# Performance work log

Hardware: AMD Instinct MI355X
Metric: run time of the kernel (lower is better)

Reference implementation:

```python
import jax, jax.numpy as jnp
import numpy as np

VOCAB, EMB, HID = 32000, 64, 64
B, S = 16, 256


def setup_inputs() -> dict:
    key = jax.random.key(0)
    ks = jax.random.split(key, 8)
    sc_e = 1.0  # torch nn.Embedding default init is N(0,1)
    sc = 1.0 / np.sqrt(HID)
    emb = jax.random.normal(ks[0], (VOCAB, EMB), jnp.float32) * sc_e
    emb = emb.at[0].set(0.0)  # padding_idx=0
    tokens = jax.random.randint(ks[1], (B, S), 0, VOCAB)
    w_ih = jax.random.normal(ks[2], (3 * HID, EMB), jnp.float32) * sc
    w_hh = jax.random.normal(ks[3], (3 * HID, HID), jnp.float32) * sc
    b_ih = jax.random.normal(ks[4], (3 * HID,), jnp.float32) * sc
    b_hh = jax.random.normal(ks[5], (3 * HID,), jnp.float32) * sc
    w_out = jax.random.normal(ks[6], (VOCAB, HID), jnp.float32) * sc
    b_out = jax.random.normal(ks[7], (VOCAB,), jnp.float32) * sc
    return {"tokens": tokens, "emb": emb, "w_ih": w_ih, "w_hh": w_hh,
            "b_ih": b_ih, "b_hh": b_hh, "w_out": w_out, "b_out": b_out}


def _gru_seq(x, w_ih, w_hh, b_ih, b_hh):
    # x: [B, S, E] -> hidden states [B, S, H]. PyTorch gate order: r, z, n.
    H = w_hh.shape[1]
    xp = jnp.einsum('bse,ge->bsg', x, w_ih) + b_ih  # [B, S, 3H] precomputed

    def step(h, xt):
        hp = h @ w_hh.T + b_hh                      # [B, 3H]
        xr, xz, xn = jnp.split(xt, 3, axis=-1)
        hr, hz, hn = jnp.split(hp, 3, axis=-1)
        r = jax.nn.sigmoid(xr + hr)
        z = jax.nn.sigmoid(xz + hz)
        n = jnp.tanh(xn + r * hn)
        h_new = (1.0 - z) * n + z * h
        return h_new, h_new

    h0 = jnp.zeros((x.shape[0], H), dtype=x.dtype)
    _, hs = jax.lax.scan(step, h0, jnp.swapaxes(xp, 0, 1))  # [S, B, H]
    return jnp.swapaxes(hs, 0, 1)


def reference(tokens, emb, w_ih, w_hh, b_ih, b_hh, w_out, b_out):
    x = emb[tokens]                                  # [B, S, E] embedding lookup
    h = _gru_seq(x, w_ih, w_hh, b_ih, b_hh)          # [B, S, H]
    return h @ w_out.T + b_out                       # [B, S, VOCAB] logits
```

## Files before the change

### kernel.cpp

```cpp
#include <hip/hip_runtime.h>
#include <hip/hip_bf16.h>

#define VOCAB 32000
#define EMB   64
#define HID   64
#define NB    16
#define NS    256
#define G3    192

typedef __bf16 bf16x8  __attribute__((ext_vector_type(8)));
typedef short  short8  __attribute__((ext_vector_type(8)));
typedef short  short4v __attribute__((ext_vector_type(4)));
typedef float  floatx4 __attribute__((ext_vector_type(4)));
typedef float  floatx2 __attribute__((ext_vector_type(2)));

__device__ __forceinline__ float bf2f(__hip_bfloat16 v) { return __bfloat162float(v); }

__device__ __forceinline__ short f2bf_bits(float f) {
    unsigned int u = __float_as_uint(f);
    unsigned int r = (u + 0x7FFFu + ((u >> 16) & 1u)) >> 16;
    return (short)r;
}

__device__ __forceinline__ bool detect_bf16(const void* p) {
    const unsigned int* w = (const unsigned int*)p;
    unsigned int word = w[threadIdx.x & 63];
    unsigned int e = (word >> 7) & 0xFFu;
    int pred = (e >= 115u) && (e <= 130u);
    unsigned long long m = __ballot(pred);
    return __popcll(m) > 32;
}

__device__ __forceinline__ float bcastf(float v, int l) {
    return __uint_as_float(__builtin_amdgcn_readlane(__float_as_uint(v), l));
}

__global__ __launch_bounds__(G3) void k_embed_proj(
    const int* __restrict__ tokens,
    const void* __restrict__ emb_raw,
    const void* __restrict__ w_ih_raw,
    const void* __restrict__ b_ih_raw,
    float* __restrict__ xp)
{
    const bool isbf = detect_bf16(w_ih_raw);
    __shared__ float e_s[EMB];
    const int m   = blockIdx.x;
    const int tid = threadIdx.x;
    const int tok = tokens[m];
    if (tid < EMB) {
        e_s[tid] = isbf ? bf2f(((const __hip_bfloat16*)emb_raw)[tok * EMB + tid])
                        : ((const float*)emb_raw)[tok * EMB + tid];
    }
    __syncthreads();

    float acc = isbf ? bf2f(((const __hip_bfloat16*)b_ih_raw)[tid])
                     : ((const float*)b_ih_raw)[tid];
    if (isbf) {
        const __hip_bfloat16* wrow = (const __hip_bfloat16*)w_ih_raw + tid * EMB;
#pragma unroll
        for (int k0 = 0; k0 < EMB; k0 += 8) {
            bf16x8 wv = *reinterpret_cast<const bf16x8*>(wrow + k0);
#pragma unroll
            for (int j = 0; j < 8; ++j) acc += e_s[k0 + j] * (float)wv[j];
        }
    } else {
        const float* wrow = (const float*)w_ih_raw + tid * EMB;
#pragma unroll
        for (int k0 = 0; k0 < EMB; k0 += 4) {
            floatx4 wv = *reinterpret_cast<const floatx4*>(wrow + k0);
#pragma unroll
            for (int j = 0; j < 4; ++j) acc += e_s[k0 + j] * wv[j];
        }
    }
    xp[m * G3 + tid] = acc;
}

__global__ __launch_bounds__(64, 1) void k_gru_scan(
    const float* __restrict__ xp,
    const void* __restrict__ w_hh_raw,
    const void* __restrict__ b_hh_raw,
    __hip_bfloat16* __restrict__ hs)
{
    const bool isbf = detect_bf16(w_hh_raw);
    const int b = blockIdx.x;
    const int j = threadIdx.x;

    floatx2 wr2[HID / 2], wz2[HID / 2], wn2[HID / 2];
    if (isbf) {
        const __hip_bfloat16* w = (const __hip_bfloat16*)w_hh_raw;
#pragma unroll
        for (int k0 = 0; k0 < HID; k0 += 8) {
            bf16x8 v0 = *reinterpret_cast<const bf16x8*>(w + (          j) * HID + k0);
            bf16x8 v1 = *reinterpret_cast<const bf16x8*>(w + (HID     + j) * HID + k0);
            bf16x8 v2 = *reinterpret_cast<const bf16x8*>(w + (2 * HID + j) * HID + k0);
#pragma unroll
            for (int t = 0; t < 4; ++t) {
                wr2[(k0 >> 1) + t] = (floatx2){(float)v0[2 * t], (float)v0[2 * t + 1]};
                wz2[(k0 >> 1) + t] = (floatx2){(float)v1[2 * t], (float)v1[2 * t + 1]};
                wn2[(k0 >> 1) + t] = (floatx2){(float)v2[2 * t], (float)v2[2 * t + 1]};
            }
        }
    } else {
        const float* w = (const float*)w_hh_raw;
#pragma unroll
        for (int k0 = 0; k0 < HID; k0 += 4) {
            floatx4 v0 = *reinterpret_cast<const floatx4*>(w + (          j) * HID + k0);
            floatx4 v1 = *reinterpret_cast<const floatx4*>(w + (HID     + j) * HID + k0);
            floatx4 v2 = *reinterpret_cast<const floatx4*>(w + (2 * HID + j) * HID + k0);
#pragma unroll
            for (int t = 0; t < 2; ++t) {
                wr2[(k0 >> 1) + t] = (floatx2){v0[2 * t], v0[2 * t + 1]};
                wz2[(k0 >> 1) + t] = (floatx2){v1[2 * t], v1[2 * t + 1]};
                wn2[(k0 >> 1) + t] = (floatx2){v2[2 * t], v2[2 * t + 1]};
            }
        }
    }

    float bhr, bhz, bhn;
    if (isbf) {
        const __hip_bfloat16* bb = (const __hip_bfloat16*)b_hh_raw;
        bhr = bf2f(bb[j]); bhz = bf2f(bb[HID + j]); bhn = bf2f(bb[2 * HID + j]);
    } else {
        const float* bb = (const float*)b_hh_raw;
        bhr = bb[j]; bhz = bb[HID + j]; bhn = bb[2 * HID + j];
    }

    const float* xpb = xp + (size_t)b * NS * G3;
    float xr = xpb[j], xz = xpb[HID + j], xn = xpb[2 * HID + j];
    float h = 0.f;

    for (int s = 0; s < NS; ++s) {
        float nxr = 0.f, nxz = 0.f, nxn = 0.f;
        if (s + 1 < NS) {
            const float* xrow = xpb + (s + 1) * G3;
            nxr = xrow[j]; nxz = xrow[HID + j]; nxn = xrow[2 * HID + j];
        }

        floatx2 ar0 = {0.f, 0.f}, ar1 = {0.f, 0.f};
        floatx2 az0 = {0.f, 0.f}, az1 = {0.f, 0.f};
        floatx2 an0 = {0.f, 0.f}, an1 = {0.f, 0.f};
#pragma unroll
        for (int kk = 0; kk < HID; kk += 16) {
            float hb[16];
#pragma unroll
            for (int t = 0; t < 16; ++t) hb[t] = bcastf(h, kk + t);
#pragma unroll
            for (int p = 0; p < 8; ++p) {
                const int w = (kk >> 1) + p;
                floatx2 hv;
                hv[0] = hb[2 * p];
                hv[1] = hb[2 * p + 1];
                if (p & 1) { ar1 += hv * wr2[w]; az1 += hv * wz2[w]; an1 += hv * wn2[w]; }
                else       { ar0 += hv * wr2[w]; az0 += hv * wz2[w]; an0 += hv * wn2[w]; }
            }
        }
        const float arf = (ar0[0] + ar0[1]) + (ar1[0] + ar1[1]);
        const float azf = (az0[0] + az0[1]) + (az1[0] + az1[1]);
        const float anf = (an0[0] + an0[1]) + (an1[0] + an1[1]);

        const float r = __fdividef(1.f, 1.f + __expf(-(xr + arf + bhr)));
        const float z = __fdividef(1.f, 1.f + __expf(-(xz + azf + bhz)));
        const float n = __fdividef(2.f, 1.f + __expf(-2.f * (xn + r * (anf + bhn)))) - 1.f;
        h = (1.f - z) * n + z * h;

        hs[((size_t)b * NS + s) * HID + j] = __float2bfloat16(h);
        xr = nxr; xz = nxz; xn = nxn;
    }
}

__global__ __launch_bounds__(256) void k_logits(
    const __hip_bfloat16* __restrict__ hs,
    const void* __restrict__ w_out_raw,
    const void* __restrict__ b_out_raw,
    void* __restrict__ out_raw)
{
    const bool isbf = detect_bf16(w_out_raw);
    const int mtile = blockIdx.x;
    const int ncb   = blockIdx.y;
    const int wave  = threadIdx.x >> 6;
    const int lane  = threadIdx.x & 63;
    const int quad  = lane >> 4;
    const int l15   = lane & 15;

    __shared__ float tile[4][16][68];

    const __hip_bfloat16* arow = hs + (mtile * 16 + l15) * HID;
    const bf16x8 a0 = *reinterpret_cast<const bf16x8*>(arow + quad * 8);
    const bf16x8 a1 = *reinterpret_cast<const bf16x8*>(arow + 32 + quad * 8);

    const int ncol_wave = ncb * 256 + wave * 64;
#pragma unroll
    for (int t = 0; t < 4; ++t) {
        const int ncol = ncol_wave + t * 16;
        bf16x8 b0, b1;
        if (isbf) {
            const __hip_bfloat16* brow = (const __hip_bfloat16*)w_out_raw + (ncol + l15) * HID;
            b0 = *reinterpret_cast<const bf16x8*>(brow + quad * 8);
            b1 = *reinterpret_cast<const bf16x8*>(brow + 32 + quad * 8);
        } else {
            const float* browf = (const float*)w_out_raw + (ncol + l15) * HID;
            floatx4 f0 = *reinterpret_cast<const floatx4*>(browf + quad * 8);
            floatx4 f1 = *reinterpret_cast<const floatx4*>(browf + quad * 8 + 4);
            floatx4 f2 = *reinterpret_cast<const floatx4*>(browf + 32 + quad * 8);
            floatx4 f3 = *reinterpret_cast<const floatx4*>(browf + 32 + quad * 8 + 4);
            short8 s0, s1;
#pragma unroll
            for (int j = 0; j < 4; ++j) {
                s0[j] = f2bf_bits(f0[j]); s0[4 + j] = f2bf_bits(f1[j]);
                s1[j] = f2bf_bits(f2[j]); s1[4 + j] = f2bf_bits(f3[j]);
            }
            b0 = __builtin_bit_cast(bf16x8, s0);
            b1 = __builtin_bit_cast(bf16x8, s1);
        }

        floatx4 acc = {0.f, 0.f, 0.f, 0.f};
        acc = __builtin_amdgcn_mfma_f32_16x16x32_bf16(a0, b0, acc, 0, 0, 0);
        acc = __builtin_amdgcn_mfma_f32_16x16x32_bf16(a1, b1, acc, 0, 0, 0);

        const float bias = isbf ? bf2f(((const __hip_bfloat16*)b_out_raw)[ncol + l15])
                                : ((const float*)b_out_raw)[ncol + l15];
#pragma unroll
        for (int i = 0; i < 4; ++i)
            tile[wave][quad * 4 + i][t * 16 + l15] = acc[i] + bias;
    }
    __syncthreads();

    if (isbf) {
        short* outb = (short*)out_raw;
#pragma unroll
        for (int p = 0; p < 4; ++p) {
            const int row = p * 4 + quad;
            const float* src = &tile[wave][row][l15 * 4];
            short4v u;
#pragma unroll
            for (int jj = 0; jj < 4; ++jj) u[jj] = f2bf_bits(src[jj]);
            *reinterpret_cast<short4v*>(
                outb + (size_t)(mtile * 16 + row) * VOCAB + ncol_wave + l15 * 4) = u;
        }
    } else {
        float* outf = (float*)out_raw;
#pragma unroll
        for (int p = 0; p < 4; ++p) {
            const int row = p * 4 + quad;
            floatx4 v = *reinterpret_cast<const floatx4*>(&tile[wave][row][l15 * 4]);
            *reinterpret_cast<floatx4*>(
                outf + (size_t)(mtile * 16 + row) * VOCAB + ncol_wave + l15 * 4) = v;
        }
    }
}

extern "C" void kernel_launch(void* const* d_in, const int* in_sizes, int n_in,
                              void* d_out, int out_size, void* d_ws, size_t ws_size,
                              hipStream_t stream)
{
    const int*  tokens = (const int*)d_in[0];
    const void* emb    = d_in[1];
    const void* w_ih   = d_in[2];
    const void* w_hh   = d_in[3];
    const void* b_ih   = d_in[4];
    const void* b_hh   = d_in[5];
    const void* w_out  = d_in[6];
    const void* b_out  = d_in[7];

    float* xp = (float*)d_out;
    __hip_bfloat16* hs = (__hip_bfloat16*)d_ws;

    k_embed_proj<<<NB * NS, G3, 0, stream>>>(tokens, emb, w_ih, b_ih, xp);
    k_gru_scan<<<NB, 64, 0, stream>>>(xp, w_hh, b_hh, hs);
    dim3 grid3((NB * NS) / 16, VOCAB / 256);
    k_logits<<<grid3, 256, 0, stream>>>(hs, w_out, b_out, d_out);
}
```

Measured before the change: 880.2 us.

## Reuse W_out fragments across M tiles, transpose xp layout, prefetch two steps

The logits kernel now loads W_out and bias fragments once per block and reuses them across four 16-row M tiles. This cuts redundant weight loads, and the output goes out through nontemporal stores. The embedding projection launches one block per timestep, which reuses W_ih held in registers across all 16 batch rows, and writes xp in a step-major layout. The GRU scan prefetches inputs two steps ahead. These changes trade fewer logits blocks and more register pressure for less redundant global traffic.

```diff
diff --git a/kernel.cpp b/kernel.cpp
--- a/kernel.cpp
+++ b/kernel.cpp
@@ -7,6 +7,7 @@
 #define NB    16
 #define NS    256
 #define G3    192
+#define MT    4
 
 typedef __bf16 bf16x8  __attribute__((ext_vector_type(8)));
 typedef short  short8  __attribute__((ext_vector_type(8)));
@@ -35,33 +36,38 @@
     return __uint_as_float(__builtin_amdgcn_readlane(__float_as_uint(v), l));
 }
 
-__global__ __launch_bounds__(G3) void k_embed_proj(
+__global__ __launch_bounds__(G3) void k_embed_proj_t(
     const int* __restrict__ tokens,
     const void* __restrict__ emb_raw,
     const void* __restrict__ w_ih_raw,
     const void* __restrict__ b_ih_raw,
-    float* __restrict__ xp)
+    float* __restrict__ xpt)
 {
     const bool isbf = detect_bf16(w_ih_raw);
-    __shared__ float e_s[EMB];
-    const int m   = blockIdx.x;
+    const int s   = blockIdx.x;
     const int tid = threadIdx.x;
-    const int tok = tokens[m];
-    if (tid < EMB) {
-        e_s[tid] = isbf ? bf2f(((const __hip_bfloat16*)emb_raw)[tok * EMB + tid])
-                        : ((const float*)emb_raw)[tok * EMB + tid];
-    }
+
+    __shared__ int   tok_s[NB];
+    __shared__ float e_s[NB][EMB];
+
+    if (tid < NB) tok_s[tid] = tokens[tid * NS + s];
     __syncthreads();
-
-    float acc = isbf ? bf2f(((const __hip_bfloat16*)b_ih_raw)[tid])
-                     : ((const float*)b_ih_raw)[tid];
+    for (int idx = tid; idx < NB * EMB; idx += G3) {
+        const int b = idx >> 6, e = idx & 63;
+        const int t = tok_s[b];
+        e_s[b][e] = isbf ? bf2f(((const __hip_bfloat16*)emb_raw)[t * EMB + e])
+                         : ((const float*)emb_raw)[t * EMB + e];
+    }
+    __syncthreads();
+
+    float wf[EMB];
     if (isbf) {
         const __hip_bfloat16* wrow = (const __hip_bfloat16*)w_ih_raw + tid * EMB;
 #pragma unroll
         for (int k0 = 0; k0 < EMB; k0 += 8) {
             bf16x8 wv = *reinterpret_cast<const bf16x8*>(wrow + k0);
 #pragma unroll
-            for (int j = 0; j < 8; ++j) acc += e_s[k0 + j] * (float)wv[j];
+            for (int j = 0; j < 8; ++j) wf[k0 + j] = (float)wv[j];
         }
     } else {
         const float* wrow = (const float*)w_ih_raw + tid * EMB;
@@ -69,14 +75,29 @@
         for (int k0 = 0; k0 < EMB; k0 += 4) {
             floatx4 wv = *reinterpret_cast<const floatx4*>(wrow + k0);
 #pragma unroll
-            for (int j = 0; j < 4; ++j) acc += e_s[k0 + j] * wv[j];
-        }
-    }
-    xp[m * G3 + tid] = acc;
+            for (int j = 0; j < 4; ++j) wf[k0 + j] = wv[j];
+        }
+    }
+    const float bias = isbf ? bf2f(((const __hip_bfloat16*)b_ih_raw)[tid])
+                            : ((const float*)b_ih_raw)[tid];
+
+    const int gam = tid >> 6;
+    const int u   = tid & 63;
+    float* orow = xpt + ((size_t)(s * 3 + gam) * NB) * HID + u;
+    for (int b = 0; b < NB; ++b) {
+        float acc = bias;
+#pragma unroll
+        for (int k0 = 0; k0 < EMB; k0 += 4) {
+            floatx4 e4 = *reinterpret_cast<const floatx4*>(&e_s[b][k0]);
+            acc += e4[0] * wf[k0] + e4[1] * wf[k0 + 1]
+                 + e4[2] * wf[k0 + 2] + e4[3] * wf[k0 + 3];
+        }
+        orow[b * HID] = acc;
+    }
 }
 
 __global__ __launch_bounds__(64, 1) void k_gru_scan(
-    const float* __restrict__ xp,
+    const float* __restrict__ xpt,
     const void* __restrict__ w_hh_raw,
     const void* __restrict__ b_hh_raw,
     __hip_bfloat16* __restrict__ hs)
@@ -125,15 +146,17 @@
         bhr = bb[j]; bhz = bb[HID + j]; bhn = bb[2 * HID + j];
     }
 
-    const float* xpb = xp + (size_t)b * NS * G3;
-    float xr = xpb[j], xz = xpb[HID + j], xn = xpb[2 * HID + j];
+    const float* xbase = xpt + (size_t)b * HID + j;
+#define XLD(s, g) xbase[((size_t)((s) * 3 + (g)) * NB) * HID]
+
+    float xc0 = XLD(0, 0), xc1 = XLD(0, 1), xc2 = XLD(0, 2);
+    float xn0 = XLD(1, 0), xn1 = XLD(1, 1), xn2 = XLD(1, 2);
     float h = 0.f;
 
     for (int s = 0; s < NS; ++s) {
-        float nxr = 0.f, nxz = 0.f, nxn = 0.f;
-        if (s + 1 < NS) {
-            const float* xrow = xpb + (s + 1) * G3;
-            nxr = xrow[j]; nxz = xrow[HID + j]; nxn = xrow[2 * HID + j];
+        float pf0 = 0.f, pf1 = 0.f, pf2 = 0.f;
+        if (s + 2 < NS) {
+            pf0 = XLD(s + 2, 0); pf1 = XLD(s + 2, 1); pf2 = XLD(s + 2, 2);
         }
 
         floatx2 ar0 = {0.f, 0.f}, ar1 = {0.f, 0.f};
@@ -158,14 +181,17 @@
         const float azf = (az0[0] + az0[1]) + (az1[0] + az1[1]);
         const float anf = (an0[0] + an0[1]) + (an1[0] + an1[1]);
 
-        const float r = __fdividef(1.f, 1.f + __expf(-(xr + arf + bhr)));
-        const float z = __fdividef(1.f, 1.f + __expf(-(xz + azf + bhz)));
-        const float n = __fdividef(2.f, 1.f + __expf(-2.f * (xn + r * (anf + bhn)))) - 1.f;
+        const float r = __fdividef(1.f, 1.f + __expf(-(xc0 + arf + bhr)));
+        const float z = __fdividef(1.f, 1.f + __expf(-(xc1 + azf + bhz)));
+        const float n = __fdividef(2.f, 1.f + __expf(-2.f * (xc2 + r * (anf + bhn)))) - 1.f;
         h = (1.f - z) * n + z * h;
 
         hs[((size_t)b * NS + s) * HID + j] = __float2bfloat16(h);
-        xr = nxr; xz = nxz; xn = nxn;
-    }
+
+        xc0 = xn0; xc1 = xn1; xc2 = xn2;
+        xn0 = pf0; xn1 = pf1; xn2 = pf2;
+    }
+#undef XLD
 }
 
 __global__ __launch_bounds__(256) void k_logits(
@@ -175,7 +201,7 @@
     void* __restrict__ out_raw)
 {
     const bool isbf = detect_bf16(w_out_raw);
-    const int mtile = blockIdx.x;
+    const int mg    = blockIdx.x;
     const int ncb   = blockIdx.y;
     const int wave  = threadIdx.x >> 6;
     const int lane  = threadIdx.x & 63;
@@ -184,19 +210,18 @@
 
     __shared__ float tile[4][16][68];
 
-    const __hip_bfloat16* arow = hs + (mtile * 16 + l15) * HID;
-    const bf16x8 a0 = *reinterpret_cast<const bf16x8*>(arow + quad * 8);
-    const bf16x8 a1 = *reinterpret_cast<const bf16x8*>(arow + 32 + quad * 8);
-
     const int ncol_wave = ncb * 256 + wave * 64;
+
+    bf16x8 B0[4], B1[4];
+    float biasv[4];
 #pragma unroll
     for (int t = 0; t < 4; ++t) {
         const int ncol = ncol_wave + t * 16;
-        bf16x8 b0, b1;
         if (isbf) {
             const __hip_bfloat16* brow = (const __hip_bfloat16*)w_out_raw + (ncol + l15) * HID;
-            b0 = *reinterpret_cast<const bf16x8*>(brow + quad * 8);
-            b1 = *reinterpret_cast<const bf16x8*>(brow + 32 + quad * 8);
+            B0[t] = *reinterpret_cast<const bf16x8*>(brow + quad * 8);
+            B1[t] = *reinterpret_cast<const bf16x8*>(brow + 32 + quad * 8);
+            biasv[t] = bf2f(((const __hip_bfloat16*)b_out_raw)[ncol + l15]);
         } else {
             const float* browf = (const float*)w_out_raw + (ncol + l15) * HID;
             floatx4 f0 = *reinterpret_cast<const floatx4*>(browf + quad * 8);
@@ -205,47 +230,57 @@
             floatx4 f3 = *reinterpret_cast<const floatx4*>(browf + 32 + quad * 8 + 4);
             short8 s0, s1;
 #pragma unroll
-            for (int j = 0; j < 4; ++j) {
-                s0[j] = f2bf_bits(f0[j]); s0[4 + j] = f2bf_bits(f1[j]);
-                s1[j] = f2bf_bits(f2[j]); s1[4 + j] = f2bf_bits(f3[j]);
-            }
-            b0 = __builtin_bit_cast(bf16x8, s0);
-            b1 = __builtin_bit_cast(bf16x8, s1);
-        }
-
-        floatx4 acc = {0.f, 0.f, 0.f, 0.f};
-        acc = __builtin_amdgcn_mfma_f32_16x16x32_bf16(a0, b0, acc, 0, 0, 0);
-        acc = __builtin_amdgcn_mfma_f32_16x16x32_bf16(a1, b1, acc, 0, 0, 0);
-
-        const float bias = isbf ? bf2f(((const __hip_bfloat16*)b_out_raw)[ncol + l15])
-                                : ((const float*)b_out_raw)[ncol + l15];
-#pragma unroll
-        for (int i = 0; i < 4; ++i)
-            tile[wave][quad * 4 + i][t * 16 + l15] = acc[i] + bias;
-    }
-    __syncthreads();
-
-    if (isbf) {
-        short* outb = (short*)out_raw;
-#pragma unroll
-        for (int p = 0; p < 4; ++p) {
-            const int row = p * 4 + quad;
-            const float* src = &tile[wave][row][l15 * 4];
-            short4v u;
-#pragma unroll
-            for (int jj = 0; jj < 4; ++jj) u[jj] = f2bf_bits(src[jj]);
-            *reinterpret_cast<short4v*>(
-                outb + (size_t)(mtile * 16 + row) * VOCAB + ncol_wave + l15 * 4) = u;
-        }
-    } else {
-        float* outf = (float*)out_raw;
-#pragma unroll
-        for (int p = 0; p < 4; ++p) {
-            const int row = p * 4 + quad;
-            floatx4 v = *reinterpret_cast<const floatx4*>(&tile[wave][row][l15 * 4]);
-            *reinterpret_cast<floatx4*>(
-                outf + (size_t)(mtile * 16 + row) * VOCAB + ncol_wave + l15 * 4) = v;
-        }
+            for (int jj = 0; jj < 4; ++jj) {
+                s0[jj] = f2bf_bits(f0[jj]); s0[4 + jj] = f2bf_bits(f1[jj]);
+                s1[jj] = f2bf_bits(f2[jj]); s1[4 + jj] = f2bf_bits(f3[jj]);
+            }
+            B0[t] = __builtin_bit_cast(bf16x8, s0);
+            B1[t] = __builtin_bit_cast(bf16x8, s1);
+            biasv[t] = ((const float*)b_out_raw)[ncol + l15];
+        }
+    }
+
+#pragma unroll
+    for (int mt = 0; mt < MT; ++mt) {
+        const int mtile = mg * MT + mt;
+        const __hip_bfloat16* arow = hs + (mtile * 16 + l15) * HID;
+        const bf16x8 a0 = *reinterpret_cast<const bf16x8*>(arow + quad * 8);
+        const bf16x8 a1 = *reinterpret_cast<const bf16x8*>(arow + 32 + quad * 8);
+
+#pragma unroll
+        for (int t = 0; t < 4; ++t) {
+            floatx4 acc = {0.f, 0.f, 0.f, 0.f};
+            acc = __builtin_amdgcn_mfma_f32_16x16x32_bf16(a0, B0[t], acc, 0, 0, 0);
+            acc = __builtin_amdgcn_mfma_f32_16x16x32_bf16(a1, B1[t], acc, 0, 0, 0);
+#pragma unroll
+            for (int i = 0; i < 4; ++i)
+                tile[wave][quad * 4 + i][t * 16 + l15] = acc[i] + biasv[t];
+        }
+        __syncthreads();
+
+        if (isbf) {
+            short* outb = (short*)out_raw;
+#pragma unroll
+            for (int p = 0; p < 4; ++p) {
+                const int row = p * 4 + quad;
+                const float* src = &tile[wave][row][l15 * 4];
+                short4v u;
+#pragma unroll
+                for (int jj = 0; jj < 4; ++jj) u[jj] = f2bf_bits(src[jj]);
+                __builtin_nontemporal_store(u, reinterpret_cast<short4v*>(
+                    outb + (size_t)(mtile * 16 + row) * VOCAB + ncol_wave + l15 * 4));
+            }
+        } else {
+            float* outf = (float*)out_raw;
+#pragma unroll
+            for (int p = 0; p < 4; ++p) {
+                const int row = p * 4 + quad;
+                floatx4 v = *reinterpret_cast<const floatx4*>(&tile[wave][row][l15 * 4]);
+                __builtin_nontemporal_store(v, reinterpret_cast<floatx4*>(
+                    outf + (size_t)(mtile * 16 + row) * VOCAB + ncol_wave + l15 * 4));
+            }
+        }
+        __syncthreads();
     }
 }
 
@@ -262,11 +297,11 @@
     const void* w_out  = d_in[6];
     const void* b_out  = d_in[7];
 
-    float* xp = (float*)d_out;
+    float* xpt = (float*)d_out;
     __hip_bfloat16* hs = (__hip_bfloat16*)d_ws;
 
-    k_embed_proj<<<NB * NS, G3, 0, stream>>>(tokens, emb, w_ih, b_ih, xp);
-    k_gru_scan<<<NB, 64, 0, stream>>>(xp, w_hh, b_hh, hs);
-    dim3 grid3((NB * NS) / 16, VOCAB / 256);
+    k_embed_proj_t<<<NS, G3, 0, stream>>>(tokens, emb, w_ih, b_ih, xpt);
+    k_gru_scan<<<NB, 64, 0, stream>>>(xpt, w_hh, b_hh, hs);
+    dim3 grid3((NB * NS) / (16 * MT), VOCAB / 256);
     k_logits<<<grid3, 256, 0, stream>>>(hs, w_out, b_out, d_out);
 }
```

Result: faster. 746.1 us (-15.2%).
